# Performance work log

Hardware: AMD Instinct MI355X
Metric: run time of the kernel (lower is better)

Reference implementation:

```python
import jax, jax.numpy as jnp
import numpy as np

GROUPS = 32
EPS = 1e-5

def group_norm(x, gamma, beta):
    B, C, H, W = x.shape
    xg = x.reshape(B, GROUPS, C // GROUPS, H, W)
    mean = xg.mean(axis=(2, 3, 4), keepdims=True)
    var = xg.var(axis=(2, 3, 4), keepdims=True)
    xn = ((xg - mean) * jax.lax.rsqrt(var + EPS)).reshape(B, C, H, W)
    return xn * gamma[None, :, None, None] + beta[None, :, None, None]

def conv1x1(x, w, b):
    # x: [B,C,H,W], w: [O,C], b: [O]
    return jnp.einsum('oc,bchw->bohw', w, x) + b[None, :, None, None]

def setup_inputs() -> dict:
    C = 256
    B, H, W = 32, 32, 32
    key = jax.random.key(0)
    ks = jax.random.split(key, 12)
    s = 0.02
    return {
        'x': jax.random.normal(ks[0], (B, C, H, W), jnp.float32),
        'gn_gamma': jnp.ones((C,), jnp.float32),
        'gn_beta': jnp.zeros((C,), jnp.float32),
        'w_qkv': jax.random.normal(ks[1], (3 * C, C), jnp.float32) * s,
        'b_qkv': jnp.zeros((3 * C,), jnp.float32),
        'w_proj': jax.random.normal(ks[2], (C, C), jnp.float32) * s,
        'b_proj': jnp.zeros((C,), jnp.float32),
        'w_se1': jax.random.normal(ks[3], (C // 4, C), jnp.float32) * s,
        'b_se1': jnp.zeros((C // 4,), jnp.float32),
        'w_se2': jax.random.normal(ks[4], (C, C // 4), jnp.float32) * s,
        'b_se2': jnp.zeros((C,), jnp.float32),
    }

def reference(x, gn_gamma, gn_beta, w_qkv, b_qkv, w_proj, b_proj, w_se1, b_se1, w_se2, b_se2):
    B, C, H, W = x.shape
    N = H * W
    residual = x
    xn = group_norm(x, gn_gamma, gn_beta)
    qkv = conv1x1(xn, w_qkv, b_qkv)            # [B,3C,H,W]
    q, k, v = jnp.split(qkv.reshape(B, 3 * C, N), 3, axis=1)  # each [B,C,N]
    scale = 1.0 / jnp.sqrt(jnp.float32(C))
    scores = jnp.einsum('bcn,bcm->bnm', q, k) * scale          # [B,N,N]
    attn = jax.nn.softmax(scores, axis=-1)
    # torch.bmm(v, attn^T): out[b,c,i] = sum_j v[b,c,j] * attn[b,i,j]
    x_attn = jnp.einsum('bcj,bij->bci', v, attn).reshape(B, C, H, W)
    x_attn = conv1x1(x_attn, w_proj, b_proj)
    # SE channel attention on the ORIGINAL x
    pooled = x.mean(axis=(2, 3))                               # [B,C]
    h1 = jax.nn.relu(pooled @ w_se1.T + b_se1)                 # [B,C//4]
    gate = jax.nn.sigmoid(h1 @ w_se2.T + b_se2)                # [B,C]
    return residual + x_attn * gate[:, :, None, None]
```

## Files before the change

kernel.cpp:

```cpp
#include <hip/hip_runtime.h>

typedef unsigned short u16;
typedef unsigned int u32;
typedef unsigned long long u64;
typedef __attribute__((ext_vector_type(4))) float vfloat4;
typedef __attribute__((ext_vector_type(16))) float vfloat16;
typedef __attribute__((ext_vector_type(8))) short vshort8;
typedef __attribute__((ext_vector_type(4))) short vshort4;
typedef __attribute__((ext_vector_type(4))) u32 vuint4;

#define DEV __device__ __forceinline__

DEV u16 f2b(float f){
  u32 u = __builtin_bit_cast(u32, f);
  u = (u + 0x7fffu + ((u >> 16) & 1u)) >> 16;
  return (u16)u;
}

typedef __attribute__((address_space(3))) u32 as3u;
typedef __attribute__((address_space(1))) u32 as1u;
DEV void gll16(const u16* g, const u16* l){
  __builtin_amdgcn_global_load_lds((const as1u*)(u64)(uintptr_t)g,
                                   (as3u*)(u32)(u64)(uintptr_t)l, 16, 0, 0);
}

__global__ void k_stats(const float* __restrict__ x, float* __restrict__ osum, float* __restrict__ osq){
  int row = blockIdx.x;
  const vfloat4* xr = (const vfloat4*)(x + (size_t)row * 1024);
  vfloat4 v = xr[threadIdx.x];
  float s = v[0]+v[1]+v[2]+v[3];
  float q = v[0]*v[0]+v[1]*v[1]+v[2]*v[2]+v[3]*v[3];
  #pragma unroll
  for (int m = 1; m < 64; m <<= 1){ s += __shfl_xor(s, m); q += __shfl_xor(q, m); }
  __shared__ float ls[4], lq[4];
  int w = threadIdx.x >> 6;
  if ((threadIdx.x & 63) == 0){ ls[w] = s; lq[w] = q; }
  __syncthreads();
  if (threadIdx.x == 0){
    osum[row] = ls[0]+ls[1]+ls[2]+ls[3];
    osq[row]  = lq[0]+lq[1]+lq[2]+lq[3];
  }
}

__global__ void k_prep(const float* __restrict__ sum, const float* __restrict__ sq,
                       const float* __restrict__ gamma, const float* __restrict__ beta,
                       const float* __restrict__ w_se1, const float* __restrict__ b_se1,
                       const float* __restrict__ w_se2, const float* __restrict__ b_se2,
                       float* __restrict__ a_scale, float* __restrict__ bsh, float* __restrict__ gate){
  int b = blockIdx.x, c = threadIdx.x;
  __shared__ float ssh[256], qsh[256], pooled[256], h1[64], meang[32], rstdg[32];
  float s = sum[b*256 + c], q = sq[b*256 + c];
  ssh[c] = s; qsh[c] = q; pooled[c] = s * (1.f/1024.f);
  __syncthreads();
  if (c < 32){
    float gs = 0.f, gq = 0.f;
    #pragma unroll
    for (int i = 0; i < 8; i++){ gs += ssh[c*8+i]; gq += qsh[c*8+i]; }
    float mean = gs * (1.f/8192.f);
    float var  = gq * (1.f/8192.f) - mean*mean;
    meang[c] = mean; rstdg[c] = rsqrtf(var + 1e-5f);
  }
  __syncthreads();
  float rs = rstdg[c>>3], mn = meang[c>>3], g = gamma[c];
  a_scale[b*256+c] = rs*g;
  bsh[b*256+c]     = beta[c] - mn*rs*g;
  if (c < 64){
    float acc = b_se1[c];
    const float* wr = w_se1 + c*256;
    for (int i = 0; i < 256; i++) acc += pooled[i]*wr[i];
    h1[c] = fmaxf(acc, 0.f);
  }
  __syncthreads();
  float acc = b_se2[c];
  const float* wr2 = w_se2 + c*64;
  #pragma unroll
  for (int j = 0; j < 64; j++) acc += h1[j]*wr2[j];
  gate[b*256+c] = 1.f / (1.f + __expf(-acc));
}

__global__ void k_wcvt(const float* __restrict__ wq, const float* __restrict__ wp,
                       u16* __restrict__ wqb, u16* __restrict__ wpb){
  int i = blockIdx.x*256 + threadIdx.x;
  if (i < 196608) wqb[i] = f2b(wq[i]);
  else            wpb[i-196608] = f2b(wp[i-196608]);
}

__global__ void k_xt(const float* __restrict__ x, const float* __restrict__ a_s,
                     const float* __restrict__ bsh, u16* __restrict__ xs_t){
  __shared__ float t[64][65];
  int b = blockIdx.z, c0 = blockIdx.y*64, n0 = blockIdx.x*64;
  int tid = threadIdx.x;
  int rr = tid >> 4, cc = (tid & 15)*4;
  #pragma unroll
  for (int itr = 0; itr < 4; itr++){
    int r = rr + itr*16;
    int c = c0 + r;
    float a = a_s[b*256 + c], bs = bsh[b*256 + c];
    vfloat4 v = *(const vfloat4*)(x + ((size_t)(b*256 + c))*1024 + n0 + cc);
    t[r][cc]   = v[0]*a + bs;
    t[r][cc+1] = v[1]*a + bs;
    t[r][cc+2] = v[2]*a + bs;
    t[r][cc+3] = v[3]*a + bs;
  }
  __syncthreads();
  int cl = tid & 63, rg = tid >> 6;
  #pragma unroll
  for (int it2 = 0; it2 < 16; it2++){
    int nl = rg*16 + it2;
    xs_t[((size_t)b*1024 + n0 + nl)*256 + c0 + cl] = f2b(t[cl][nl]);
  }
}

__global__ __launch_bounds__(256) void k_qkv(
    const u16* __restrict__ wq_b, const u16* __restrict__ xs_t,
    const float* __restrict__ b_qkv,
    u16* __restrict__ qt, u16* __restrict__ kph, u16* __restrict__ vph){
  __shared__ u16 Alds[128*40];
  __shared__ u16 Blds[128*40];
  int bid = blockIdx.x;
  int xcd = bid & 7, idx = bid >> 3;
  int b   = xcd*4 + idx/48;
  int rem = idx % 48;
  int o0 = (rem >> 3) * 128;
  int n0 = (rem & 7) * 128;
  int tid = threadIdx.x;
  int w = tid >> 6, lane = tid & 63, lo = lane & 15, hi = lane >> 4;
  int wr = w >> 1, wc = w & 1;
  vfloat4 acc[4][4];
  #pragma unroll
  for (int i = 0; i < 4; i++)
    #pragma unroll
    for (int j = 0; j < 4; j++) acc[i][j] = vfloat4{0.f,0.f,0.f,0.f};

  for (int ks = 0; ks < 8; ks++){
    int c0 = ks*32;
    __syncthreads();
    #pragma unroll
    for (int i = 0; i < 2; i++){
      int cid = tid + i*256;
      int row = cid >> 2, h4 = cid & 3;
      vshort8 a = *(const vshort8*)(wq_b + (o0+row)*256 + c0 + h4*8);
      *(vshort8*)(Alds + row*40 + h4*8) = a;
      vshort8 bl = *(const vshort8*)(xs_t + ((size_t)b*1024 + n0 + row)*256 + c0 + h4*8);
      *(vshort8*)(Blds + row*40 + h4*8) = bl;
    }
    __syncthreads();
    vshort8 af[4], bf[4];
    #pragma unroll
    for (int of = 0; of < 4; of++) af[of] = *(const vshort8*)(Alds + (wr*64+of*16+lo)*40 + hi*8);
    #pragma unroll
    for (int nf = 0; nf < 4; nf++) bf[nf] = *(const vshort8*)(Blds + (wc*64+nf*16+lo)*40 + hi*8);
    #pragma unroll
    for (int of = 0; of < 4; of++)
      #pragma unroll
      for (int nf = 0; nf < 4; nf++)
        acc[of][nf] = __builtin_amdgcn_mfma_f32_16x16x32_bf16(af[of], bf[nf], acc[of][nf], 0, 0, 0);
  }

  int kind = o0 >> 8;
  #pragma unroll
  for (int of = 0; of < 4; of++){
    int ob = o0 + wr*64 + of*16 + hi*4;
    vfloat4 bq = *(const vfloat4*)(b_qkv + ob);
    #pragma unroll
    for (int nf = 0; nf < 4; nf++){
      int n = n0 + wc*64 + nf*16 + lo;
      int tile = n >> 5, j = n & 31;
      vfloat4 val = acc[of][nf];
      #pragma unroll
      for (int r = 0; r < 4; r++) val[r] += bq[r];
      if (kind == 0){
        vshort4 p;
        #pragma unroll
        for (int r = 0; r < 4; r++) p[r] = (short)f2b(val[r] * 0.09016844f);
        *(vshort4*)(qt + ((size_t)b*1024 + n)*256 + ob) = p;
      } else if (kind == 1){
        vshort4 p;
        #pragma unroll
        for (int r = 0; r < 4; r++) p[r] = (short)f2b(val[r]);
        int cx = ob - 256;
        int slot = (cx >> 3) ^ j;
        *(vshort4*)(kph + ((size_t)b << 18) + tile*8192 + j*256 + slot*8 + (cx & 7)) = p;
      } else {
        int m2 = (j >> 4) & 1, q2 = (j >> 2) & 1;
        int e2 = (j & 3) | ((j & 8) >> 1);
        #pragma unroll
        for (int r = 0; r < 4; r++){
          int c = ob - 512 + r;
          int a2 = c >> 2;
          int off = a2*128 + (c & 3)*32 + ((((m2 << 1) | q2) ^ (a2 & 3)) << 3) + e2;
          vph[((size_t)b << 18) + tile*8192 + off] = f2b(val[r]);
        }
      }
    }
  }
}

__global__ __launch_bounds__(256, 1) void k_attn(
    const u16* __restrict__ qt, const u16* __restrict__ kph, const u16* __restrict__ vph,
    const u16* __restrict__ wp_b, const float* __restrict__ b_proj,
    const float* __restrict__ gate, const float* __restrict__ x,
    float* __restrict__ out){
  __shared__ u16 smem[33792];
  int bid = blockIdx.x;
  int xcd = bid & 7, idx = bid >> 3;
  int b = xcd*4 + (idx >> 3);
  int i0 = (idx & 7) * 128;
  int tid = threadIdx.x, w = tid >> 6, lane = tid & 63, lo = lane & 15, hi = lane >> 4;
  int jj = lane & 31, q = lane >> 5;

  int iq = i0 + w*32 + jj;
  vshort8 qf[16];
  #pragma unroll
  for (int kk = 0; kk < 16; kk++)
    qf[kk] = *(const vshort8*)(qt + ((size_t)b*1024 + iq)*256 + kk*16 + q*8);

  vfloat16 Oacc[8];
  #pragma unroll
  for (int ct = 0; ct < 8; ct++)
    #pragma unroll
    for (int e = 0; e < 16; e++) Oacc[ct][e] = 0.f;
  float m_run = -1e30f, l_run = 0.f;

  int koff[16];
  #pragma unroll
  for (int kk = 0; kk < 16; kk++)
    koff[kk] = jj*256 + ((((kk << 1) | q) ^ jj) << 3);
  int a0 = jj >> 2;
  int vb = a0*128 + (jj & 3)*32;
  int xm0 = ((q)       ^ (a0 & 3)) << 3;
  int xm1 = ((2 | q)   ^ (a0 & 3)) << 3;

  const u16* kbat = kph + ((size_t)b << 18);
  const u16* vbat = vph + ((size_t)b << 18);

  auto STAGE = [&](int tt, int buf){
    const u16* ks = kbat + (size_t)tt * 8192;
    const u16* vs = vbat + (size_t)tt * 8192;
    u16* kd = smem + buf * 8192;
    u16* vd = smem + 16384 + buf * 8192;
    #pragma unroll
    for (int s = 0; s < 4; s++){
      int ch = (s*256 + tid) * 8;
      gll16(ks + ch, kd + ch);
      gll16(vs + ch, vd + ch);
    }
  };

  STAGE(0, 0);
  __syncthreads();

  for (int t = 0; t < 32; t++){
    int buf = t & 1;
    if (t < 31) STAGE(t + 1, buf ^ 1);
    const u16* Kb = smem + buf*8192;
    const u16* Vb = smem + 16384 + buf*8192;

    vfloat16 stA, stB;
    #pragma unroll
    for (int e = 0; e < 16; e++){ stA[e] = 0.f; stB[e] = 0.f; }
    __builtin_amdgcn_s_setprio(1);
    #pragma unroll
    for (int kk = 0; kk < 16; kk += 2){
      vshort8 k0 = *(const vshort8*)(Kb + koff[kk]);
      vshort8 k1 = *(const vshort8*)(Kb + koff[kk+1]);
      stA = __builtin_amdgcn_mfma_f32_32x32x16_bf16(k0, qf[kk],   stA, 0,0,0);
      stB = __builtin_amdgcn_mfma_f32_32x32x16_bf16(k1, qf[kk+1], stB, 0,0,0);
    }
    __builtin_amdgcn_s_setprio(0);
    vfloat16 st = stA + stB;

    float pml = st[0];
    #pragma unroll
    for (int e = 1; e < 16; e++) pml = fmaxf(pml, st[e]);
    if (!__all(pml - m_run <= 8.f)){
      float po = fmaxf(pml, __shfl_xor(pml, 32));
      float mn = fmaxf(m_run, po);
      float corr = exp2f(m_run - mn);
      #pragma unroll
      for (int ct = 0; ct < 8; ct++) Oacc[ct] *= corr;
      l_run *= corr;
      m_run = mn;
    }

    float pv[16]; float ls = 0.f;
    #pragma unroll
    for (int e = 0; e < 16; e++){ pv[e] = exp2f(st[e] - m_run); ls += pv[e]; }
    l_run += ls;

    u32 pw[8];
    #pragma unroll
    for (int rr = 0; rr < 4; rr++){
      asm("v_cvt_pk_bf16_f32 %0, %1, %2" : "=v"(pw[rr])   : "v"(pv[2*rr]),   "v"(pv[2*rr+1]));
      asm("v_cvt_pk_bf16_f32 %0, %1, %2" : "=v"(pw[4+rr]) : "v"(pv[8+2*rr]), "v"(pv[8+2*rr+1]));
    }
    vshort8 pf0 = __builtin_bit_cast(vshort8, vuint4{pw[0], pw[1], pw[2], pw[3]});
    vshort8 pf1 = __builtin_bit_cast(vshort8, vuint4{pw[4], pw[5], pw[6], pw[7]});

    __builtin_amdgcn_s_setprio(1);
    #pragma unroll
    for (int ct = 0; ct < 8; ct++){
      vshort8 v0 = *(const vshort8*)(Vb + ct*1024 + vb + xm0);
      vshort8 v1 = *(const vshort8*)(Vb + ct*1024 + vb + xm1);
      Oacc[ct] = __builtin_amdgcn_mfma_f32_32x32x16_bf16(v0, pf0, Oacc[ct], 0,0,0);
      Oacc[ct] = __builtin_amdgcn_mfma_f32_32x32x16_bf16(v1, pf1, Oacc[ct], 0,0,0);
    }
    __builtin_amdgcn_s_setprio(0);
    __syncthreads();
  }

  float lt = l_run + __shfl_xor(l_run, 32);
  float inv = 1.f / lt;

  __syncthreads();
  u16* Ol = smem;
  #pragma unroll
  for (int ct = 0; ct < 8; ct++)
    #pragma unroll
    for (int qd = 0; qd < 4; qd++){
      vshort4 pk;
      #pragma unroll
      for (int e3 = 0; e3 < 4; e3++) pk[e3] = (short)f2b(Oacc[ct][4*qd + e3] * inv);
      int cb = ct*32 + 8*qd + 4*q;
      *(vshort4*)(Ol + (w*32 + jj)*264 + cb) = pk;
    }
  __syncthreads();

  vfloat4 acc2[4][8];
  #pragma unroll
  for (int i = 0; i < 4; i++)
    #pragma unroll
    for (int j = 0; j < 8; j++) acc2[i][j] = vfloat4{0.f,0.f,0.f,0.f};
  #pragma unroll
  for (int ct = 0; ct < 8; ct++){
    vshort8 wf[4], ofr[8];
    #pragma unroll
    for (int o4 = 0; o4 < 4; o4++)
      wf[o4] = *(const vshort8*)(wp_b + (w*64 + o4*16 + lo)*256 + ct*32 + hi*8);
    #pragma unroll
    for (int i4 = 0; i4 < 8; i4++)
      ofr[i4] = *(const vshort8*)(Ol + (i4*16 + lo)*264 + ct*32 + hi*8);
    #pragma unroll
    for (int o4 = 0; o4 < 4; o4++)
      #pragma unroll
      for (int i4 = 0; i4 < 8; i4++)
        acc2[o4][i4] = __builtin_amdgcn_mfma_f32_16x16x32_bf16(wf[o4], ofr[i4], acc2[o4][i4], 0,0,0);
  }

  #pragma unroll
  for (int o4 = 0; o4 < 4; o4++){
    int ob = w*64 + o4*16 + hi*4;
    vfloat4 bp = *(const vfloat4*)(b_proj + ob);
    vfloat4 gt = *(const vfloat4*)(gate + b*256 + ob);
    #pragma unroll
    for (int i4 = 0; i4 < 8; i4++){
      int n = i0 + i4*16 + lo;
      #pragma unroll
      for (int e = 0; e < 4; e++){
        size_t idxo = ((size_t)(b*256) + ob + e)*1024 + n;
        out[idxo] = x[idxo] + (acc2[o4][i4][e] + bp[e]) * gt[e];
      }
    }
  }
}

extern "C" void kernel_launch(void* const* d_in, const int* in_sizes, int n_in,
                              void* d_out, int out_size, void* d_ws, size_t ws_size,
                              hipStream_t stream){
  const float* x      = (const float*)d_in[0];
  const float* gamma  = (const float*)d_in[1];
  const float* beta   = (const float*)d_in[2];
  const float* w_qkv  = (const float*)d_in[3];
  const float* b_qkv  = (const float*)d_in[4];
  const float* w_proj = (const float*)d_in[5];
  const float* b_proj = (const float*)d_in[6];
  const float* w_se1  = (const float*)d_in[7];
  const float* b_se1  = (const float*)d_in[8];
  const float* w_se2  = (const float*)d_in[9];
  const float* b_se2  = (const float*)d_in[10];
  float* out = (float*)d_out;
  char* ws = (char*)d_ws;

  float* sum  = (float*)(ws + 0);
  float* sq   = (float*)(ws + 32768);
  float* a_s  = (float*)(ws + 65536);
  float* bsh  = (float*)(ws + 98304);
  float* gate = (float*)(ws + 131072);
  u16* wq_b   = (u16*)(ws + 163840);
  u16* wp_b   = (u16*)(ws + 557056);
  u16* xs_t   = (u16*)(ws + 688128);
  u16* qt     = (u16*)(ws + 17465344);
  u16* kph    = (u16*)(ws + 34242560);
  u16* vph    = (u16*)(ws + 51019776);

  k_stats<<<8192, 256, 0, stream>>>(x, sum, sq);
  k_wcvt <<<1024, 256, 0, stream>>>(w_qkv, w_proj, wq_b, wp_b);
  k_prep <<<32,   256, 0, stream>>>(sum, sq, gamma, beta, w_se1, b_se1, w_se2, b_se2, a_s, bsh, gate);
  k_xt   <<<dim3(16,4,32), 256, 0, stream>>>(x, a_s, bsh, xs_t);
  k_qkv  <<<1536, 256, 0, stream>>>(wq_b, xs_t, b_qkv, qt, kph, vph);
  k_attn <<<256,  256, 0, stream>>>(qt, kph, vph, wp_b, b_proj, gate, x, out);
}
```

Measured before the change: 120.0 us.

## Split attention KV sequence across wave pairs with in-block softmax merge

Doubles the attention block to 512 threads. Each pair of waves shares a 32-query row, and each wave in the pair processes alternate key/value tiles, staging two tiles per round into a larger shared buffer. The partial softmax states are merged through shared memory (max, sum and a bf16-rounded partial O), and the projection epilogue is split across 8 waves. The aim is more waves per CU to hide MFMA and LDS latency on a grid of only 256 blocks. The cost is extra LDS, more register pressure under launch_bounds(512,2), and an added rounding of the partial output to bf16.

```diff
diff --git a/kernel.cpp b/kernel.cpp
--- a/kernel.cpp
+++ b/kernel.cpp
@@ -16,6 +16,7 @@
   u = (u + 0x7fffu + ((u >> 16) & 1u)) >> 16;
   return (u16)u;
 }
+DEV float b2f(u16 h){ u32 u = ((u32)h) << 16; return __builtin_bit_cast(float, u); }
 
 typedef __attribute__((address_space(3))) u32 as3u;
 typedef __attribute__((address_space(1))) u32 as1u;
@@ -196,20 +197,22 @@
   }
 }
 
-__global__ __launch_bounds__(256, 1) void k_attn(
+__global__ __launch_bounds__(512, 2) void k_attn(
     const u16* __restrict__ qt, const u16* __restrict__ kph, const u16* __restrict__ vph,
     const u16* __restrict__ wp_b, const float* __restrict__ b_proj,
     const float* __restrict__ gate, const float* __restrict__ x,
     float* __restrict__ out){
-  __shared__ u16 smem[33792];
+  __shared__ u16 smem[65536];
+  __shared__ float Ml[8][32], Ll[8][32];
   int bid = blockIdx.x;
   int xcd = bid & 7, idx = bid >> 3;
   int b = xcd*4 + (idx >> 3);
   int i0 = (idx & 7) * 128;
   int tid = threadIdx.x, w = tid >> 6, lane = tid & 63, lo = lane & 15, hi = lane >> 4;
   int jj = lane & 31, q = lane >> 5;
-
-  int iq = i0 + w*32 + jj;
+  int r = w >> 1, g = w & 1;
+
+  int iq = i0 + r*32 + jj;
   vshort8 qf[16];
   #pragma unroll
   for (int kk = 0; kk < 16; kk++)
@@ -228,33 +231,33 @@
     koff[kk] = jj*256 + ((((kk << 1) | q) ^ jj) << 3);
   int a0 = jj >> 2;
   int vb = a0*128 + (jj & 3)*32;
-  int xm0 = ((q)       ^ (a0 & 3)) << 3;
-  int xm1 = ((2 | q)   ^ (a0 & 3)) << 3;
+  int xm0 = ((q)     ^ (a0 & 3)) << 3;
+  int xm1 = ((2 | q) ^ (a0 & 3)) << 3;
 
   const u16* kbat = kph + ((size_t)b << 18);
   const u16* vbat = vph + ((size_t)b << 18);
 
-  auto STAGE = [&](int tt, int buf){
-    const u16* ks = kbat + (size_t)tt * 8192;
-    const u16* vs = vbat + (size_t)tt * 8192;
-    u16* kd = smem + buf * 8192;
-    u16* vd = smem + 16384 + buf * 8192;
-    #pragma unroll
-    for (int s = 0; s < 4; s++){
-      int ch = (s*256 + tid) * 8;
-      gll16(ks + ch, kd + ch);
-      gll16(vs + ch, vd + ch);
+  auto STAGE = [&](int rd, int buf){
+    #pragma unroll
+    for (int s = 0; s < 8; s++){
+      int cid = s*512 + tid;
+      int arr = cid >> 11;
+      int tt  = (cid >> 10) & 1;
+      int ch  = (cid & 1023) * 8;
+      const u16* src = (arr ? vbat : kbat) + (size_t)(2*rd + tt)*8192 + ch;
+      u16* dst = smem + arr*32768 + buf*16384 + tt*8192 + ch;
+      gll16(src, dst);
     }
   };
 
   STAGE(0, 0);
   __syncthreads();
 
-  for (int t = 0; t < 32; t++){
-    int buf = t & 1;
-    if (t < 31) STAGE(t + 1, buf ^ 1);
-    const u16* Kb = smem + buf*8192;
-    const u16* Vb = smem + 16384 + buf*8192;
+  for (int rd = 0; rd < 16; rd++){
+    int buf = rd & 1;
+    if (rd < 15) STAGE(rd + 1, buf ^ 1);
+    const u16* Kb = smem + buf*16384 + g*8192;
+    const u16* Vb = smem + 32768 + buf*16384 + g*8192;
 
     vfloat16 stA, stB;
     #pragma unroll
@@ -310,46 +313,73 @@
   }
 
   float lt = l_run + __shfl_xor(l_run, 32);
-  float inv = 1.f / lt;
-
-  __syncthreads();
-  u16* Ol = smem;
-  #pragma unroll
-  for (int ct = 0; ct < 8; ct++)
-    #pragma unroll
-    for (int qd = 0; qd < 4; qd++){
-      vshort4 pk;
-      #pragma unroll
-      for (int e3 = 0; e3 < 4; e3++) pk[e3] = (short)f2b(Oacc[ct][4*qd + e3] * inv);
-      int cb = ct*32 + 8*qd + 4*q;
-      *(vshort4*)(Ol + (w*32 + jj)*264 + cb) = pk;
-    }
-  __syncthreads();
-
-  vfloat4 acc2[4][8];
-  #pragma unroll
-  for (int i = 0; i < 4; i++)
+
+  if (q == 0){ Ml[w][jj] = m_run; Ll[w][jj] = lt; }
+  __syncthreads();
+  int pw2 = w ^ 1;
+  float mp = Ml[pw2][jj], lp = Ll[pw2][jj];
+  float mm = fmaxf(m_run, mp);
+  float sc = exp2f(m_run - mm);
+  float l_tot = lt * sc + lp * exp2f(mp - mm);
+  float inv = 1.f / l_tot;
+  #pragma unroll
+  for (int ct = 0; ct < 8; ct++) Oacc[ct] *= sc;
+  __syncthreads();
+
+  u16* Ox = smem;
+  if (g == 1){
+    #pragma unroll
+    for (int ct = 0; ct < 8; ct++)
+      #pragma unroll
+      for (int qd = 0; qd < 4; qd++){
+        vshort4 pk;
+        #pragma unroll
+        for (int e3 = 0; e3 < 4; e3++) pk[e3] = (short)f2b(Oacc[ct][4*qd + e3]);
+        int cb = ct*32 + 8*qd + 4*q;
+        *(vshort4*)(Ox + (r*32 + jj)*264 + cb) = pk;
+      }
+  }
+  __syncthreads();
+  if (g == 0){
+    #pragma unroll
+    for (int ct = 0; ct < 8; ct++)
+      #pragma unroll
+      for (int qd = 0; qd < 4; qd++){
+        int cb = ct*32 + 8*qd + 4*q;
+        vshort4 pp = *(const vshort4*)(Ox + (r*32 + jj)*264 + cb);
+        vshort4 po;
+        #pragma unroll
+        for (int e3 = 0; e3 < 4; e3++)
+          po[e3] = (short)f2b((Oacc[ct][4*qd + e3] + b2f((u16)pp[e3])) * inv);
+        *(vshort4*)(Ox + (r*32 + jj)*264 + cb) = po;
+      }
+  }
+  __syncthreads();
+
+  vfloat4 acc2[2][8];
+  #pragma unroll
+  for (int i = 0; i < 2; i++)
     #pragma unroll
     for (int j = 0; j < 8; j++) acc2[i][j] = vfloat4{0.f,0.f,0.f,0.f};
   #pragma unroll
   for (int ct = 0; ct < 8; ct++){
-    vshort8 wf[4], ofr[8];
-    #pragma unroll
-    for (int o4 = 0; o4 < 4; o4++)
-      wf[o4] = *(const vshort8*)(wp_b + (w*64 + o4*16 + lo)*256 + ct*32 + hi*8);
+    vshort8 wf[2], ofr[8];
+    #pragma unroll
+    for (int o4 = 0; o4 < 2; o4++)
+      wf[o4] = *(const vshort8*)(wp_b + (w*32 + o4*16 + lo)*256 + ct*32 + hi*8);
     #pragma unroll
     for (int i4 = 0; i4 < 8; i4++)
-      ofr[i4] = *(const vshort8*)(Ol + (i4*16 + lo)*264 + ct*32 + hi*8);
-    #pragma unroll
-    for (int o4 = 0; o4 < 4; o4++)
+      ofr[i4] = *(const vshort8*)(Ox + (i4*16 + lo)*264 + ct*32 + hi*8);
+    #pragma unroll
+    for (int o4 = 0; o4 < 2; o4++)
       #pragma unroll
       for (int i4 = 0; i4 < 8; i4++)
         acc2[o4][i4] = __builtin_amdgcn_mfma_f32_16x16x32_bf16(wf[o4], ofr[i4], acc2[o4][i4], 0,0,0);
   }
 
   #pragma unroll
-  for (int o4 = 0; o4 < 4; o4++){
-    int ob = w*64 + o4*16 + hi*4;
+  for (int o4 = 0; o4 < 2; o4++){
+    int ob = w*32 + o4*16 + hi*4;
     vfloat4 bp = *(const vfloat4*)(b_proj + ob);
     vfloat4 gt = *(const vfloat4*)(gate + b*256 + ob);
     #pragma unroll
@@ -398,5 +428,5 @@
   k_prep <<<32,   256, 0, stream>>>(sum, sq, gamma, beta, w_se1, b_se1, w_se2, b_se2, a_s, bsh, gate);
   k_xt   <<<dim3(16,4,32), 256, 0, stream>>>(x, a_s, bsh, xs_t);
   k_qkv  <<<1536, 256, 0, stream>>>(wq_b, xs_t, b_qkv, qt, kph, vph);
-  k_attn <<<256,  256, 0, stream>>>(qt, kph, vph, wp_b, b_proj, gate, x, out);
-}
+  k_attn <<<256,  512, 0, stream>>>(qt, kph, vph, wp_b, b_proj, gate, x, out);
+}
```

Result: slower. 135.2 us (+12.7%).

## Process two key/value tiles per iteration in attention main loop

Applied to the files above, without the earlier changes.

The flash-attention loop now stages two 32-key K/V tiles per round instead of one. This halves the number of rounds and block-wide barriers and does one online-softmax max/rescale check per 64 keys. It also issues more independent MFMAs between barriers. In exchange, shared memory per block grows to 128 KB and register pressure rises with the extra score accumulators and probability fragments.

```diff
diff --git a/kernel.cpp b/kernel.cpp
--- a/kernel.cpp
+++ b/kernel.cpp
@@ -201,7 +201,7 @@
     const u16* __restrict__ wp_b, const float* __restrict__ b_proj,
     const float* __restrict__ gate, const float* __restrict__ x,
     float* __restrict__ out){
-  __shared__ u16 smem[33792];
+  __shared__ u16 smem[65536];
   int bid = blockIdx.x;
   int xcd = bid & 7, idx = bid >> 3;
   int b = xcd*4 + (idx >> 3);
@@ -228,51 +228,60 @@
     koff[kk] = jj*256 + ((((kk << 1) | q) ^ jj) << 3);
   int a0 = jj >> 2;
   int vb = a0*128 + (jj & 3)*32;
-  int xm0 = ((q)       ^ (a0 & 3)) << 3;
-  int xm1 = ((2 | q)   ^ (a0 & 3)) << 3;
+  int xm0 = ((q)     ^ (a0 & 3)) << 3;
+  int xm1 = ((2 | q) ^ (a0 & 3)) << 3;
 
   const u16* kbat = kph + ((size_t)b << 18);
   const u16* vbat = vph + ((size_t)b << 18);
 
-  auto STAGE = [&](int tt, int buf){
-    const u16* ks = kbat + (size_t)tt * 8192;
-    const u16* vs = vbat + (size_t)tt * 8192;
-    u16* kd = smem + buf * 8192;
-    u16* vd = smem + 16384 + buf * 8192;
-    #pragma unroll
-    for (int s = 0; s < 4; s++){
-      int ch = (s*256 + tid) * 8;
-      gll16(ks + ch, kd + ch);
-      gll16(vs + ch, vd + ch);
+  auto STAGE = [&](int rd, int buf){
+    #pragma unroll
+    for (int s = 0; s < 16; s++){
+      int cid = s*256 + tid;
+      int arr = cid >> 11;
+      int tt  = (cid >> 10) & 1;
+      int ch  = (cid & 1023) * 8;
+      const u16* src = (arr ? vbat : kbat) + (size_t)(2*rd + tt)*8192 + ch;
+      u16* dst = smem + arr*32768 + buf*16384 + tt*8192 + ch;
+      gll16(src, dst);
     }
   };
 
   STAGE(0, 0);
   __syncthreads();
 
-  for (int t = 0; t < 32; t++){
-    int buf = t & 1;
-    if (t < 31) STAGE(t + 1, buf ^ 1);
-    const u16* Kb = smem + buf*8192;
-    const u16* Vb = smem + 16384 + buf*8192;
-
-    vfloat16 stA, stB;
-    #pragma unroll
-    for (int e = 0; e < 16; e++){ stA[e] = 0.f; stB[e] = 0.f; }
+  for (int rd = 0; rd < 16; rd++){
+    int buf = rd & 1;
+    if (rd < 15) STAGE(rd + 1, buf ^ 1);
+    const u16* Kb0 = smem + buf*16384;
+    const u16* Kb1 = Kb0 + 8192;
+    const u16* Vb0 = smem + 32768 + buf*16384;
+    const u16* Vb1 = Vb0 + 8192;
+
+    vfloat16 s0a, s0b, s1a, s1b;
+    #pragma unroll
+    for (int e = 0; e < 16; e++){ s0a[e]=0.f; s0b[e]=0.f; s1a[e]=0.f; s1b[e]=0.f; }
     __builtin_amdgcn_s_setprio(1);
     #pragma unroll
     for (int kk = 0; kk < 16; kk += 2){
-      vshort8 k0 = *(const vshort8*)(Kb + koff[kk]);
-      vshort8 k1 = *(const vshort8*)(Kb + koff[kk+1]);
-      stA = __builtin_amdgcn_mfma_f32_32x32x16_bf16(k0, qf[kk],   stA, 0,0,0);
-      stB = __builtin_amdgcn_mfma_f32_32x32x16_bf16(k1, qf[kk+1], stB, 0,0,0);
+      vshort8 k00 = *(const vshort8*)(Kb0 + koff[kk]);
+      vshort8 k01 = *(const vshort8*)(Kb0 + koff[kk+1]);
+      vshort8 k10 = *(const vshort8*)(Kb1 + koff[kk]);
+      vshort8 k11 = *(const vshort8*)(Kb1 + koff[kk+1]);
+      s0a = __builtin_amdgcn_mfma_f32_32x32x16_bf16(k00, qf[kk],   s0a, 0,0,0);
+      s0b = __builtin_amdgcn_mfma_f32_32x32x16_bf16(k01, qf[kk+1], s0b, 0,0,0);
+      s1a = __builtin_amdgcn_mfma_f32_32x32x16_bf16(k10, qf[kk],   s1a, 0,0,0);
+      s1b = __builtin_amdgcn_mfma_f32_32x32x16_bf16(k11, qf[kk+1], s1b, 0,0,0);
     }
     __builtin_amdgcn_s_setprio(0);
-    vfloat16 st = stA + stB;
-
-    float pml = st[0];
-    #pragma unroll
-    for (int e = 1; e < 16; e++) pml = fmaxf(pml, st[e]);
+    vfloat16 st0 = s0a + s0b;
+    vfloat16 st1 = s1a + s1b;
+
+    float pml = st0[0];
+    #pragma unroll
+    for (int e = 1; e < 16; e++) pml = fmaxf(pml, st0[e]);
+    #pragma unroll
+    for (int e = 0; e < 16; e++) pml = fmaxf(pml, st1[e]);
     if (!__all(pml - m_run <= 8.f)){
       float po = fmaxf(pml, __shfl_xor(pml, 32));
       float mn = fmaxf(m_run, po);
@@ -283,27 +292,37 @@
       m_run = mn;
     }
 
-    float pv[16]; float ls = 0.f;
-    #pragma unroll
-    for (int e = 0; e < 16; e++){ pv[e] = exp2f(st[e] - m_run); ls += pv[e]; }
+    float pv0[16], pv1[16]; float ls = 0.f;
+    #pragma unroll
+    for (int e = 0; e < 16; e++){ pv0[e] = exp2f(st0[e] - m_run); ls += pv0[e]; }
+    #pragma unroll
+    for (int e = 0; e < 16; e++){ pv1[e] = exp2f(st1[e] - m_run); ls += pv1[e]; }
     l_run += ls;
 
-    u32 pw[8];
+    u32 pw0[8], pw1[8];
     #pragma unroll
     for (int rr = 0; rr < 4; rr++){
-      asm("v_cvt_pk_bf16_f32 %0, %1, %2" : "=v"(pw[rr])   : "v"(pv[2*rr]),   "v"(pv[2*rr+1]));
-      asm("v_cvt_pk_bf16_f32 %0, %1, %2" : "=v"(pw[4+rr]) : "v"(pv[8+2*rr]), "v"(pv[8+2*rr+1]));
-    }
-    vshort8 pf0 = __builtin_bit_cast(vshort8, vuint4{pw[0], pw[1], pw[2], pw[3]});
-    vshort8 pf1 = __builtin_bit_cast(vshort8, vuint4{pw[4], pw[5], pw[6], pw[7]});
+      asm("v_cvt_pk_bf16_f32 %0, %1, %2" : "=v"(pw0[rr])   : "v"(pv0[2*rr]),   "v"(pv0[2*rr+1]));
+      asm("v_cvt_pk_bf16_f32 %0, %1, %2" : "=v"(pw0[4+rr]) : "v"(pv0[8+2*rr]), "v"(pv0[8+2*rr+1]));
+      asm("v_cvt_pk_bf16_f32 %0, %1, %2" : "=v"(pw1[rr])   : "v"(pv1[2*rr]),   "v"(pv1[2*rr+1]));
+      asm("v_cvt_pk_bf16_f32 %0, %1, %2" : "=v"(pw1[4+rr]) : "v"(pv1[8+2*rr]), "v"(pv1[8+2*rr+1]));
+    }
+    vshort8 pa0 = __builtin_bit_cast(vshort8, vuint4{pw0[0], pw0[1], pw0[2], pw0[3]});
+    vshort8 pa1 = __builtin_bit_cast(vshort8, vuint4{pw0[4], pw0[5], pw0[6], pw0[7]});
+    vshort8 pb0 = __builtin_bit_cast(vshort8, vuint4{pw1[0], pw1[1], pw1[2], pw1[3]});
+    vshort8 pb1 = __builtin_bit_cast(vshort8, vuint4{pw1[4], pw1[5], pw1[6], pw1[7]});
 
     __builtin_amdgcn_s_setprio(1);
     #pragma unroll
     for (int ct = 0; ct < 8; ct++){
-      vshort8 v0 = *(const vshort8*)(Vb + ct*1024 + vb + xm0);
-      vshort8 v1 = *(const vshort8*)(Vb + ct*1024 + vb + xm1);
-      Oacc[ct] = __builtin_amdgcn_mfma_f32_32x32x16_bf16(v0, pf0, Oacc[ct], 0,0,0);
-      Oacc[ct] = __builtin_amdgcn_mfma_f32_32x32x16_bf16(v1, pf1, Oacc[ct], 0,0,0);
+      vshort8 v00 = *(const vshort8*)(Vb0 + ct*1024 + vb + xm0);
+      vshort8 v01 = *(const vshort8*)(Vb0 + ct*1024 + vb + xm1);
+      vshort8 v10 = *(const vshort8*)(Vb1 + ct*1024 + vb + xm0);
+      vshort8 v11 = *(const vshort8*)(Vb1 + ct*1024 + vb + xm1);
+      Oacc[ct] = __builtin_amdgcn_mfma_f32_32x32x16_bf16(v00, pa0, Oacc[ct], 0,0,0);
+      Oacc[ct] = __builtin_amdgcn_mfma_f32_32x32x16_bf16(v01, pa1, Oacc[ct], 0,0,0);
+      Oacc[ct] = __builtin_amdgcn_mfma_f32_32x32x16_bf16(v10, pb0, Oacc[ct], 0,0,0);
+      Oacc[ct] = __builtin_amdgcn_mfma_f32_32x32x16_bf16(v11, pb1, Oacc[ct], 0,0,0);
     }
     __builtin_amdgcn_s_setprio(0);
     __syncthreads();
```

New measurement: 132.0 us. 10.0% more time.

## Pre-swizzle QKV GEMM operands and double-buffer via direct global-to-LDS loads

Applied to the files above, without the earlier changes.

The weight and normalized-activation buffers are now written in an XOR-swizzled channel order, so the QKV GEMM can stage 64-wide K slices straight into LDS with global_load_lds into two alternating buffers. Each slice's load overlaps the MFMA work on the previous one, and the register round-trip plus one barrier per step go away. LDS use grows to 64KB and launch bounds force one block per SIMD group, which lowers occupancy. The attention kernel is untouched apart from whitespace.

```diff
diff --git a/kernel.cpp b/kernel.cpp
--- a/kernel.cpp
+++ b/kernel.cpp
@@ -79,14 +79,19 @@
 }
 
 __global__ void k_wcvt(const float* __restrict__ wq, const float* __restrict__ wp,
-                       u16* __restrict__ wqb, u16* __restrict__ wpb){
+                       u16* __restrict__ wqs, u16* __restrict__ wpb){
   int i = blockIdx.x*256 + threadIdx.x;
-  if (i < 196608) wqb[i] = f2b(wq[i]);
-  else            wpb[i-196608] = f2b(wp[i-196608]);
+  if (i < 196608){
+    int o = i >> 8, c = i & 255;
+    int sidx = o*256 + (c & 192) + ((((c >> 3) & 7) ^ (o & 7)) << 3) + (c & 7);
+    wqs[sidx] = f2b(wq[i]);
+  } else {
+    wpb[i-196608] = f2b(wp[i-196608]);
+  }
 }
 
 __global__ void k_xt(const float* __restrict__ x, const float* __restrict__ a_s,
-                     const float* __restrict__ bsh, u16* __restrict__ xs_t){
+                     const float* __restrict__ bsh, u16* __restrict__ xss){
   __shared__ float t[64][65];
   int b = blockIdx.z, c0 = blockIdx.y*64, n0 = blockIdx.x*64;
   int tid = threadIdx.x;
@@ -107,16 +112,17 @@
   #pragma unroll
   for (int it2 = 0; it2 < 16; it2++){
     int nl = rg*16 + it2;
-    xs_t[((size_t)b*1024 + n0 + nl)*256 + c0 + cl] = f2b(t[cl][nl]);
-  }
-}
-
-__global__ __launch_bounds__(256) void k_qkv(
-    const u16* __restrict__ wq_b, const u16* __restrict__ xs_t,
+    int n = n0 + nl, c = c0 + cl;
+    int sidx = (c & 192) + ((((c >> 3) & 7) ^ (n & 7)) << 3) + (c & 7);
+    xss[((size_t)b*1024 + n)*256 + sidx] = f2b(t[cl][nl]);
+  }
+}
+
+__global__ __launch_bounds__(256, 1) void k_qkv(
+    const u16* __restrict__ wqs, const u16* __restrict__ xss,
     const float* __restrict__ b_qkv,
     u16* __restrict__ qt, u16* __restrict__ kph, u16* __restrict__ vph){
-  __shared__ u16 Alds[128*40];
-  __shared__ u16 Blds[128*40];
+  __shared__ u16 smem[32768];
   int bid = blockIdx.x;
   int xcd = bid & 7, idx = bid >> 3;
   int b   = xcd*4 + idx/48;
@@ -126,35 +132,52 @@
   int tid = threadIdx.x;
   int w = tid >> 6, lane = tid & 63, lo = lane & 15, hi = lane >> 4;
   int wr = w >> 1, wc = w & 1;
+
+  const u16* wsrc = wqs + (size_t)o0*256;
+  const u16* xsrc = xss + ((size_t)b*1024 + n0)*256;
+
+  auto STAGE = [&](int d, int buf){
+    #pragma unroll
+    for (int s = 0; s < 4; s++){
+      int cid = s*256 + tid;
+      int row = cid >> 3, slot = cid & 7;
+      int off = row*256 + d*64 + ((slot ^ (row & 7)) << 3);
+      gll16(wsrc + off, smem + buf*8192 + cid*8);
+      gll16(xsrc + off, smem + 16384 + buf*8192 + cid*8);
+    }
+  };
+
   vfloat4 acc[4][4];
   #pragma unroll
   for (int i = 0; i < 4; i++)
     #pragma unroll
     for (int j = 0; j < 4; j++) acc[i][j] = vfloat4{0.f,0.f,0.f,0.f};
 
-  for (int ks = 0; ks < 8; ks++){
-    int c0 = ks*32;
+  STAGE(0, 0);
+  __syncthreads();
+
+  for (int d = 0; d < 4; d++){
+    int buf = d & 1;
+    if (d < 3) STAGE(d+1, buf^1);
+    const u16* Al = smem + buf*8192;
+    const u16* Bl = smem + 16384 + buf*8192;
+    #pragma unroll
+    for (int ksl = 0; ksl < 2; ksl++){
+      vshort8 af[4], bf[4];
+      int xs = ((ksl*4 + hi) ^ (lo & 7)) << 3;
+      #pragma unroll
+      for (int of = 0; of < 4; of++)
+        af[of] = *(const vshort8*)(Al + (wr*64 + of*16 + lo)*64 + xs);
+      #pragma unroll
+      for (int nf = 0; nf < 4; nf++)
+        bf[nf] = *(const vshort8*)(Bl + (wc*64 + nf*16 + lo)*64 + xs);
+      #pragma unroll
+      for (int of = 0; of < 4; of++)
+        #pragma unroll
+        for (int nf = 0; nf < 4; nf++)
+          acc[of][nf] = __builtin_amdgcn_mfma_f32_16x16x32_bf16(af[of], bf[nf], acc[of][nf], 0, 0, 0);
+    }
     __syncthreads();
-    #pragma unroll
-    for (int i = 0; i < 2; i++){
-      int cid = tid + i*256;
-      int row = cid >> 2, h4 = cid & 3;
-      vshort8 a = *(const vshort8*)(wq_b + (o0+row)*256 + c0 + h4*8);
-      *(vshort8*)(Alds + row*40 + h4*8) = a;
-      vshort8 bl = *(const vshort8*)(xs_t + ((size_t)b*1024 + n0 + row)*256 + c0 + h4*8);
-      *(vshort8*)(Blds + row*40 + h4*8) = bl;
-    }
-    __syncthreads();
-    vshort8 af[4], bf[4];
-    #pragma unroll
-    for (int of = 0; of < 4; of++) af[of] = *(const vshort8*)(Alds + (wr*64+of*16+lo)*40 + hi*8);
-    #pragma unroll
-    for (int nf = 0; nf < 4; nf++) bf[nf] = *(const vshort8*)(Blds + (wc*64+nf*16+lo)*40 + hi*8);
-    #pragma unroll
-    for (int of = 0; of < 4; of++)
-      #pragma unroll
-      for (int nf = 0; nf < 4; nf++)
-        acc[of][nf] = __builtin_amdgcn_mfma_f32_16x16x32_bf16(af[of], bf[nf], acc[of][nf], 0, 0, 0);
   }
 
   int kind = o0 >> 8;
@@ -228,8 +251,8 @@
     koff[kk] = jj*256 + ((((kk << 1) | q) ^ jj) << 3);
   int a0 = jj >> 2;
   int vb = a0*128 + (jj & 3)*32;
-  int xm0 = ((q)       ^ (a0 & 3)) << 3;
-  int xm1 = ((2 | q)   ^ (a0 & 3)) << 3;
+  int xm0 = ((q)     ^ (a0 & 3)) << 3;
+  int xm1 = ((2 | q) ^ (a0 & 3)) << 3;
 
   const u16* kbat = kph + ((size_t)b << 18);
   const u16* vbat = vph + ((size_t)b << 18);
@@ -386,17 +409,17 @@
   float* a_s  = (float*)(ws + 65536);
   float* bsh  = (float*)(ws + 98304);
   float* gate = (float*)(ws + 131072);
-  u16* wq_b   = (u16*)(ws + 163840);
+  u16* wqs    = (u16*)(ws + 163840);
   u16* wp_b   = (u16*)(ws + 557056);
-  u16* xs_t   = (u16*)(ws + 688128);
+  u16* xss    = (u16*)(ws + 688128);
   u16* qt     = (u16*)(ws + 17465344);
   u16* kph    = (u16*)(ws + 34242560);
   u16* vph    = (u16*)(ws + 51019776);
 
   k_stats<<<8192, 256, 0, stream>>>(x, sum, sq);
-  k_wcvt <<<1024, 256, 0, stream>>>(w_qkv, w_proj, wq_b, wp_b);
+  k_wcvt <<<1024, 256, 0, stream>>>(w_qkv, w_proj, wqs, wp_b);
   k_prep <<<32,   256, 0, stream>>>(sum, sq, gamma, beta, w_se1, b_se1, w_se2, b_se2, a_s, bsh, gate);
-  k_xt   <<<dim3(16,4,32), 256, 0, stream>>>(x, a_s, bsh, xs_t);
-  k_qkv  <<<1536, 256, 0, stream>>>(wq_b, xs_t, b_qkv, qt, kph, vph);
+  k_xt   <<<dim3(16,4,32), 256, 0, stream>>>(x, a_s, bsh, xss);
+  k_qkv  <<<1536, 256, 0, stream>>>(wqs, xss, b_qkv, qt, kph, vph);
   k_attn <<<256,  256, 0, stream>>>(qt, kph, vph, wp_b, b_proj, gate, x, out);
 }
```

After: 127.7 us. 1.06x slower.
